# Kernel tuning notes

Measured on AMD Instinct MI355X. Metric: run time of the kernel, lower is better.

The kernel has to match this reference:

```python
import jax, jax.numpy as jnp
import numpy as np

NEG_INF = -jnp.inf  # aggregation identity for the max-plus semifield


def setup_inputs() -> dict:
    key = jax.random.key(0)
    k1, k2, k3 = jax.random.split(key, 3)
    B, C_in, C_out, H, W, M, N = 4, 32, 32, 80, 80, 5, 5
    x = jax.random.normal(k1, (B, C_in, H, W), dtype=jnp.float32)
    w = jax.random.normal(k2, (C_out, C_in, M, N), dtype=jnp.float32) * 0.1
    bias = jax.random.normal(k3, (C_out,), dtype=jnp.float32) * 0.1
    return {"x": x, "w": w, "bias": bias}


def reference(x, w, bias):
    """Max-plus semifield conv: out[b,co,h,w] = bias[co] + sum_ci max_{m,n} (x_pad[b,ci,h+m,w+n] + w[co,ci,m,n]).

    Faithful to SemiConv2d._semi_conv with semifield = (amax, add, -inf, 0),
    but computed with a running max over the MN taps instead of materializing
    the [B, C_out, C_in, M*N, H*W] tensor the torch code builds via unfold.
    """
    B, C_in, H, W = x.shape
    C_out, _, M, N = w.shape
    # padding exactly as in _semi_conv (odd vs even kernel), fill = aggregation identity
    pt, pb = (M // 2, M // 2) if M % 2 else (M // 2 - 1, M // 2)
    pl, pr = (N // 2, N // 2) if N % 2 else (N // 2 - 1, N // 2)
    xp = jnp.pad(x, ((0, 0), (0, 0), (pt, pb), (pl, pr)), constant_values=NEG_INF)
    # running max over the M*N taps (fixed small loop, not a data-dim loop)
    acc = jnp.full((B, C_out, C_in, H, W), NEG_INF, dtype=x.dtype)
    for m in range(M):
        for n in range(N):
            patch = xp[:, :, m:m + H, n:n + W]               # [B, C_in, H, W]
            tap = patch[:, None] + w[None, :, :, m, n, None, None]  # [B, C_out, C_in, H, W]
            acc = jnp.maximum(acc, tap)
    out = jnp.sum(acc, axis=2) + bias[None, :, None, None]   # sum over C_in, add bias
    return out
```

## Files before the change

### kernel.cpp

```cpp
#include <hip/hip_runtime.h>
#include <math.h>

#define CIN  32
#define COUT 32
#define BB   4
#define HH   80
#define WW   80
#define HW   (HH * WW)
#define NOUT (BB * COUT * HW)
#define TH   16
#define XR   20
#define XC   88
#define TILE (XR * XC)
#define NT   320

typedef float v4f __attribute__((ext_vector_type(4)));

__device__ __forceinline__ float max3f(float a, float b, float c) {
    float d;
    asm("v_max3_f32 %0, %1, %2, %3" : "=v"(d) : "v"(a), "v"(b), "v"(c));
    return d;
}

__device__ __forceinline__ void load_lds4(const float* g, float* l) {
    __builtin_amdgcn_global_load_lds(
        (const __attribute__((address_space(1))) void*)g,
        (__attribute__((address_space(3))) void*)l, 4, 0, 0);
}

template<int NP>
__global__ __launch_bounds__(NT, 6) void semiconv_kernel(
    const float* __restrict__ x,
    const float* __restrict__ w,
    const float* __restrict__ bias,
    float* __restrict__ dst)
{
    constexpr int CP = CIN / NP;
    __shared__ __align__(16) float xs0[TILE];
    __shared__ __align__(16) float xs1[TILE];
    __shared__ __align__(16) float wl[CP * 100];

    const int tid = threadIdx.x;
    const int bh  = blockIdx.x;
    const int cq  = blockIdx.y;
    const int zz  = blockIdx.z;
    const int b    = zz / NP;
    const int part = zz % NP;
    const int ci0  = part * CP;
    const int h0   = bh * TH;
    const int co0  = cq * 4;

    for (int idx = tid; idx < CP * 100; idx += NT) {
        int cop = idx / (CP * 25);
        int r   = idx % (CP * 25);
        int k = r / 25, t = r % 25, m = t / 5, n = t % 5;
        wl[k * 100 + m * 20 + n * 4 + cop] =
            w[((size_t)(co0 + cop) * CIN + ci0) * 25 + r];
    }

    const int ty = tid / 20, tx = tid % 20, wc = tx * 4;

    int goff[6];
    #pragma unroll
    for (int i = 0; i < 6; ++i) {
        int idx = tid + i * NT;
        int r = idx / XC, c = idx % XC;
        int gr = h0 + r - 2, gc = c - 2;
        bool in = (idx < TILE) && gr >= 0 && gr < HH && gc >= 0 && gc < WW;
        goff[i] = in ? (gr * WW + gc) : -1;
        if (idx < TILE && !in) { xs0[idx] = -INFINITY; xs1[idx] = -INFINITY; }
    }
    const bool has6 = (tid < TILE - 5 * NT);

    const float* xbase = x + (size_t)(b * CIN + ci0) * HW;
    const int wave64 = tid & ~63;

    #pragma unroll
    for (int i = 0; i < 5; ++i)
        if (goff[i] >= 0) load_lds4(xbase + goff[i], xs0 + i * NT + wave64);
    if (has6 && goff[5] >= 0) load_lds4(xbase + goff[5], xs0 + 5 * NT + wave64);

    const float* xnext = xbase + HW;
    float s[4][4];
    #pragma unroll
    for (int c = 0; c < 4; ++c)
        #pragma unroll
        for (int j = 0; j < 4; ++j) s[c][j] = 0.f;
    const int xro = ty * XC + wc;

    __syncthreads();

    auto step = [&](int k, const float* xrd, float* xwr) {
        if (k + 1 < CP) {
            #pragma unroll
            for (int i = 0; i < 5; ++i)
                if (goff[i] >= 0) load_lds4(xnext + goff[i], xwr + i * NT + wave64);
            if (has6 && goff[5] >= 0) load_lds4(xnext + goff[5], xwr + 5 * NT + wave64);
            xnext += HW;
        }
        const float* wk = &wl[k * 100];
        float acc[4][4];
        #pragma unroll
        for (int c = 0; c < 4; ++c)
            #pragma unroll
            for (int j = 0; j < 4; ++j) acc[c][j] = -INFINITY;

        #pragma unroll
        for (int m = 0; m < 5; ++m) {
            v4f A = *(const v4f*)(xrd + xro + m * XC);
            v4f C = *(const v4f*)(xrd + xro + m * XC + 4);
            float xr[8] = {A.x, A.y, A.z, A.w, C.x, C.y, C.z, C.w};
            v4f W0 = *(const v4f*)(wk + m * 20);
            v4f W1 = *(const v4f*)(wk + m * 20 + 4);
            v4f W2 = *(const v4f*)(wk + m * 20 + 8);
            v4f W3 = *(const v4f*)(wk + m * 20 + 12);
            v4f W4 = *(const v4f*)(wk + m * 20 + 16);
            float wn0[4] = {W0.x, W0.y, W0.z, W0.w};
            float wn1[4] = {W1.x, W1.y, W1.z, W1.w};
            float wn2[4] = {W2.x, W2.y, W2.z, W2.w};
            float wn3[4] = {W3.x, W3.y, W3.z, W3.w};
            float wn4[4] = {W4.x, W4.y, W4.z, W4.w};
            #pragma unroll
            for (int c = 0; c < 4; ++c) {
                #pragma unroll
                for (int j = 0; j < 4; ++j) {
                    float p0 = xr[j]     + wn0[c];
                    float p1 = xr[j + 1] + wn1[c];
                    float p2 = xr[j + 2] + wn2[c];
                    float p3 = xr[j + 3] + wn3[c];
                    float p4 = xr[j + 4] + wn4[c];
                    acc[c][j] = max3f(acc[c][j], max3f(p0, p1, p2), fmaxf(p3, p4));
                }
            }
        }
        #pragma unroll
        for (int c = 0; c < 4; ++c)
            #pragma unroll
            for (int j = 0; j < 4; ++j) s[c][j] += acc[c][j];
        __syncthreads();
    };

    #pragma unroll 1
    for (int k = 0; k < CP; k += 2) {
        step(k,     xs0, xs1);
        step(k + 1, xs1, xs0);
    }

    size_t oi = (((size_t)b * COUT + co0) * HH + (h0 + ty)) * WW + wc;
    float* o = (NP == 1) ? dst : dst + (size_t)part * NOUT;
    #pragma unroll
    for (int c = 0; c < 4; ++c) {
        float add = (NP == 1) ? bias[co0 + c] : 0.f;
        v4f r = {s[c][0] + add, s[c][1] + add, s[c][2] + add, s[c][3] + add};
        *(v4f*)(o + oi + (size_t)c * HW) = r;
    }
}

template<int NP>
__global__ __launch_bounds__(256) void reduceN_kernel(
    const float* __restrict__ ws, const float* __restrict__ bias,
    float* __restrict__ out)
{
    int i4 = blockIdx.x * 256 + threadIdx.x;
    const float4* p = reinterpret_cast<const float4*>(ws);
    float4 r = p[i4];
    #pragma unroll
    for (int q = 1; q < NP; ++q) {
        float4 t = p[i4 + (size_t)q * (NOUT / 4)];
        r.x += t.x; r.y += t.y; r.z += t.z; r.w += t.w;
    }
    int co = (i4 / (HW / 4)) & (COUT - 1);
    float bc = bias[co];
    r.x += bc; r.y += bc; r.z += bc; r.w += bc;
    reinterpret_cast<float4*>(out)[i4] = r;
}

extern "C" void kernel_launch(void* const* d_in, const int* in_sizes, int n_in,
                              void* d_out, int out_size, void* d_ws, size_t ws_size,
                              hipStream_t stream) {
    const float* x    = (const float*)d_in[0];
    const float* w    = (const float*)d_in[1];
    const float* bias = (const float*)d_in[2];
    float* out        = (float*)d_out;

    const size_t need8 = 8ull * NOUT * sizeof(float);
    const size_t need4 = 4ull * NOUT * sizeof(float);

    if (ws_size >= need8) {
        dim3 grid(HH / TH, COUT / 4, BB * 8);
        semiconv_kernel<8><<<grid, NT, 0, stream>>>(x, w, bias, (float*)d_ws);
        reduceN_kernel<8><<<NOUT / 4 / 256, 256, 0, stream>>>((const float*)d_ws, bias, out);
    } else if (ws_size >= need4) {
        dim3 grid(HH / TH, COUT / 4, BB * 4);
        semiconv_kernel<4><<<grid, NT, 0, stream>>>(x, w, bias, (float*)d_ws);
        reduceN_kernel<4><<<NOUT / 4 / 256, 256, 0, stream>>>((const float*)d_ws, bias, out);
    } else {
        dim3 grid(HH / TH, COUT / 4, BB);
        semiconv_kernel<1><<<grid, NT, 0, stream>>>(x, w, bias, out);
    }
}
```

Baseline: 44.51 us.

## Preload all channel tiles into LDS up front and drop per-channel barriers

Replaces the double-buffered per-channel LDS pipeline with a single upfront load of all CP channel tiles (4 with NP=8) into LDS, followed by one barrier and a fully unrolled compute loop with no per-step __syncthreads. The first tap row initialises the accumulator directly instead of starting from -inf. The aim is to remove the per-channel barrier and latency-exposure cost, at the price of larger LDS use per block, which may lower occupancy. The NP=1 fallback is replaced by a naive kernel, since the larger LDS footprint no longer fits that path.

```diff
diff --git a/kernel.cpp b/kernel.cpp
--- a/kernel.cpp
+++ b/kernel.cpp
@@ -32,12 +32,10 @@
 __global__ __launch_bounds__(NT, 6) void semiconv_kernel(
     const float* __restrict__ x,
     const float* __restrict__ w,
-    const float* __restrict__ bias,
     float* __restrict__ dst)
 {
     constexpr int CP = CIN / NP;
-    __shared__ __align__(16) float xs0[TILE];
-    __shared__ __align__(16) float xs1[TILE];
+    __shared__ __align__(16) float xs[CP][TILE];
     __shared__ __align__(16) float wl[CP * 100];
 
     const int tid = threadIdx.x;
@@ -50,6 +48,31 @@
     const int h0   = bh * TH;
     const int co0  = cq * 4;
 
+    const int ty = tid / 20, tx = tid % 20, wc = tx * 4;
+    const int xro = ty * XC + wc;
+
+    int goff[6];
+    #pragma unroll
+    for (int i = 0; i < 6; ++i) {
+        int idx = tid + i * NT;
+        int r = idx / XC, c = idx % XC;
+        int gr = h0 + r - 2, gc = c - 2;
+        bool in = (idx < TILE) && gr >= 0 && gr < HH && gc >= 0 && gc < WW;
+        goff[i] = in ? (gr * WW + gc) : -1;
+    }
+    const bool has6 = (tid < TILE - 5 * NT);
+
+    const float* xb0 = x + (size_t)(b * CIN + ci0) * HW;
+    const int wave64 = tid & ~63;
+    #pragma unroll
+    for (int t = 0; t < CP; ++t) {
+        const float* xp = xb0 + (size_t)t * HW;
+        #pragma unroll
+        for (int i = 0; i < 5; ++i)
+            if (goff[i] >= 0) load_lds4(xp + goff[i], &xs[t][i * NT + wave64]);
+        if (has6 && goff[5] >= 0) load_lds4(xp + goff[5], &xs[t][5 * NT + wave64]);
+    }
+
     for (int idx = tid; idx < CP * 100; idx += NT) {
         int cop = idx / (CP * 25);
         int r   = idx % (CP * 25);
@@ -58,78 +81,46 @@
             w[((size_t)(co0 + cop) * CIN + ci0) * 25 + r];
     }
 
-    const int ty = tid / 20, tx = tid % 20, wc = tx * 4;
-
-    int goff[6];
     #pragma unroll
     for (int i = 0; i < 6; ++i) {
         int idx = tid + i * NT;
-        int r = idx / XC, c = idx % XC;
-        int gr = h0 + r - 2, gc = c - 2;
-        bool in = (idx < TILE) && gr >= 0 && gr < HH && gc >= 0 && gc < WW;
-        goff[i] = in ? (gr * WW + gc) : -1;
-        if (idx < TILE && !in) { xs0[idx] = -INFINITY; xs1[idx] = -INFINITY; }
-    }
-    const bool has6 = (tid < TILE - 5 * NT);
-
-    const float* xbase = x + (size_t)(b * CIN + ci0) * HW;
-    const int wave64 = tid & ~63;
-
-    #pragma unroll
-    for (int i = 0; i < 5; ++i)
-        if (goff[i] >= 0) load_lds4(xbase + goff[i], xs0 + i * NT + wave64);
-    if (has6 && goff[5] >= 0) load_lds4(xbase + goff[5], xs0 + 5 * NT + wave64);
-
-    const float* xnext = xbase + HW;
+        if (idx < TILE && goff[i] < 0) {
+            #pragma unroll
+            for (int t = 0; t < CP; ++t) xs[t][idx] = -INFINITY;
+        }
+    }
+
     float s[4][4];
     #pragma unroll
     for (int c = 0; c < 4; ++c)
         #pragma unroll
         for (int j = 0; j < 4; ++j) s[c][j] = 0.f;
-    const int xro = ty * XC + wc;
 
     __syncthreads();
 
-    auto step = [&](int k, const float* xrd, float* xwr) {
-        if (k + 1 < CP) {
-            #pragma unroll
-            for (int i = 0; i < 5; ++i)
-                if (goff[i] >= 0) load_lds4(xnext + goff[i], xwr + i * NT + wave64);
-            if (has6 && goff[5] >= 0) load_lds4(xnext + goff[5], xwr + 5 * NT + wave64);
-            xnext += HW;
-        }
+    #pragma unroll
+    for (int k = 0; k < CP; ++k) {
+        const float* xb = &xs[k][xro];
         const float* wk = &wl[k * 100];
         float acc[4][4];
         #pragma unroll
-        for (int c = 0; c < 4; ++c)
-            #pragma unroll
-            for (int j = 0; j < 4; ++j) acc[c][j] = -INFINITY;
-
-        #pragma unroll
         for (int m = 0; m < 5; ++m) {
-            v4f A = *(const v4f*)(xrd + xro + m * XC);
-            v4f C = *(const v4f*)(xrd + xro + m * XC + 4);
-            float xr[8] = {A.x, A.y, A.z, A.w, C.x, C.y, C.z, C.w};
+            v4f A  = *(const v4f*)(xb + m * XC);
+            v4f C  = *(const v4f*)(xb + m * XC + 4);
             v4f W0 = *(const v4f*)(wk + m * 20);
             v4f W1 = *(const v4f*)(wk + m * 20 + 4);
             v4f W2 = *(const v4f*)(wk + m * 20 + 8);
             v4f W3 = *(const v4f*)(wk + m * 20 + 12);
             v4f W4 = *(const v4f*)(wk + m * 20 + 16);
-            float wn0[4] = {W0.x, W0.y, W0.z, W0.w};
-            float wn1[4] = {W1.x, W1.y, W1.z, W1.w};
-            float wn2[4] = {W2.x, W2.y, W2.z, W2.w};
-            float wn3[4] = {W3.x, W3.y, W3.z, W3.w};
-            float wn4[4] = {W4.x, W4.y, W4.z, W4.w};
+            float xr[8] = {A.x, A.y, A.z, A.w, C.x, C.y, C.z, C.w};
             #pragma unroll
             for (int c = 0; c < 4; ++c) {
+                float q0 = W0[c], q1 = W1[c], q2 = W2[c], q3 = W3[c], q4 = W4[c];
                 #pragma unroll
                 for (int j = 0; j < 4; ++j) {
-                    float p0 = xr[j]     + wn0[c];
-                    float p1 = xr[j + 1] + wn1[c];
-                    float p2 = xr[j + 2] + wn2[c];
-                    float p3 = xr[j + 3] + wn3[c];
-                    float p4 = xr[j + 4] + wn4[c];
-                    acc[c][j] = max3f(acc[c][j], max3f(p0, p1, p2), fmaxf(p3, p4));
+                    float t = max3f(xr[j] + q0, xr[j + 1] + q1, xr[j + 2] + q2);
+                    float u = fmaxf(xr[j + 3] + q3, xr[j + 4] + q4);
+                    acc[c][j] = (m == 0) ? fmaxf(t, u) : max3f(acc[c][j], t, u);
                 }
             }
         }
@@ -137,21 +128,13 @@
         for (int c = 0; c < 4; ++c)
             #pragma unroll
             for (int j = 0; j < 4; ++j) s[c][j] += acc[c][j];
-        __syncthreads();
-    };
-
-    #pragma unroll 1
-    for (int k = 0; k < CP; k += 2) {
-        step(k,     xs0, xs1);
-        step(k + 1, xs1, xs0);
     }
 
     size_t oi = (((size_t)b * COUT + co0) * HH + (h0 + ty)) * WW + wc;
-    float* o = (NP == 1) ? dst : dst + (size_t)part * NOUT;
+    float* o = dst + (size_t)part * NOUT;
     #pragma unroll
     for (int c = 0; c < 4; ++c) {
-        float add = (NP == 1) ? bias[co0 + c] : 0.f;
-        v4f r = {s[c][0] + add, s[c][1] + add, s[c][2] + add, s[c][3] + add};
+        v4f r = {s[c][0], s[c][1], s[c][2], s[c][3]};
         *(v4f*)(o + oi + (size_t)c * HW) = r;
     }
 }
@@ -175,6 +158,32 @@
     reinterpret_cast<float4*>(out)[i4] = r;
 }
 
+__global__ __launch_bounds__(256) void naive_kernel(
+    const float* __restrict__ x, const float* __restrict__ w,
+    const float* __restrict__ bias, float* __restrict__ out)
+{
+    int o = blockIdx.x * 256 + threadIdx.x;
+    if (o >= NOUT) return;
+    int wcol = o % WW, h = (o / WW) % HH, co = (o / HW) % COUT, b = o / (COUT * HW);
+    float sum = 0.f;
+    for (int ci = 0; ci < CIN; ++ci) {
+        float mx = -INFINITY;
+        for (int m = 0; m < 5; ++m) {
+            int gr = h + m - 2;
+            if (gr < 0 || gr >= HH) continue;
+            for (int n = 0; n < 5; ++n) {
+                int gc = wcol + n - 2;
+                if (gc < 0 || gc >= WW) continue;
+                float v = x[((size_t)(b * CIN + ci)) * HW + gr * WW + gc]
+                        + w[((size_t)(co * CIN + ci)) * 25 + m * 5 + n];
+                mx = fmaxf(mx, v);
+            }
+        }
+        sum += mx;
+    }
+    out[o] = sum + bias[co];
+}
+
 extern "C" void kernel_launch(void* const* d_in, const int* in_sizes, int n_in,
                               void* d_out, int out_size, void* d_ws, size_t ws_size,
                               hipStream_t stream) {
@@ -188,14 +197,13 @@
 
     if (ws_size >= need8) {
         dim3 grid(HH / TH, COUT / 4, BB * 8);
-        semiconv_kernel<8><<<grid, NT, 0, stream>>>(x, w, bias, (float*)d_ws);
+        semiconv_kernel<8><<<grid, NT, 0, stream>>>(x, w, (float*)d_ws);
         reduceN_kernel<8><<<NOUT / 4 / 256, 256, 0, stream>>>((const float*)d_ws, bias, out);
     } else if (ws_size >= need4) {
         dim3 grid(HH / TH, COUT / 4, BB * 4);
-        semiconv_kernel<4><<<grid, NT, 0, stream>>>(x, w, bias, (float*)d_ws);
+        semiconv_kernel<4><<<grid, NT, 0, stream>>>(x, w, (float*)d_ws);
         reduceN_kernel<4><<<NOUT / 4 / 256, 256, 0, stream>>>((const float*)d_ws, bias, out);
     } else {
-        dim3 grid(HH / TH, COUT / 4, BB);
-        semiconv_kernel<1><<<grid, NT, 0, stream>>>(x, w, bias, out);
-    }
-}
+        naive_kernel<<<(NOUT + 255) / 256, 256, 0, stream>>>(x, w, bias, out);
+    }
+}
```

Result: faster. 42.79 us (-3.8%).
